# Optimization experiments

Measured on AMD Instinct MI355X. Metric: run time of the kernel, lower is better.

## Reference

```python
import jax, jax.numpy as jnp
import numpy as np

N_NODES = 50000


def _add_self_loops(edge_index, n):
    loops = jnp.arange(n, dtype=edge_index.dtype)
    src = jnp.concatenate([edge_index[0], loops])
    dst = jnp.concatenate([edge_index[1], loops])
    return src, dst


def _gcn_norm(src, dst, n):
    # symmetric normalization deg^-1/2 (degrees include self-loops), as in PyG GCNConv
    ones = jnp.ones_like(dst, dtype=jnp.float32)
    deg = jax.ops.segment_sum(ones, dst, num_segments=n)
    dinv = jnp.where(deg > 0, jax.lax.rsqrt(deg), 0.0)
    return dinv[src] * dinv[dst]


def _gcn_conv(x, W, b, src, dst, norm, n):
    h = x @ W                                  # [N, d_out] dense transform first (d_out <= d_in)
    msg = h[src] * norm[:, None]               # gather + per-edge scale
    out = jax.ops.segment_sum(msg, dst, num_segments=n)  # scatter-add aggregation
    return out + b


def setup_inputs() -> dict:
    key = jax.random.key(0)
    ks = jax.random.split(key, 5)
    n, e = N_NODES, 1_600_000
    x = jax.random.normal(ks[0], (n, 512), dtype=jnp.float32)
    edge_index = jax.random.randint(ks[1], (2, e), 0, n, dtype=jnp.int64)
    def glorot(k, fi, fo):
        s = jnp.sqrt(6.0 / (fi + fo)).astype(jnp.float32)
        return jax.random.uniform(k, (fi, fo), jnp.float32, -s, s)
    return {
        "x": x,
        "edge_index": edge_index,
        "W0": glorot(ks[2], 512, 256), "b0": jnp.zeros((256,), jnp.float32),
        "W1": glorot(ks[3], 256, 256), "b1": jnp.zeros((256,), jnp.float32),
        "W2": glorot(ks[4], 256, 128), "b2": jnp.zeros((128,), jnp.float32),
    }


def reference(x, edge_index, W0, b0, W1, b1, W2, b2):
    n = x.shape[0]
    src, dst = _add_self_loops(edge_index, n)
    norm = _gcn_norm(src, dst, n)
    h = jax.nn.relu(_gcn_conv(x, W0, b0, src, dst, norm, n))
    h = jax.nn.relu(_gcn_conv(h, W1, b1, src, dst, norm, n))
    z = _gcn_conv(h, W2, b2, src, dst, norm, n)
    return z
```

## Files before the change

kernel.cpp:

```cpp
#include <hip/hip_runtime.h>
#include <hip/hip_bf16.h>
#include <type_traits>

#define NN 50000

typedef __attribute__((ext_vector_type(8))) short bf16x8;
typedef __attribute__((ext_vector_type(4))) float f32x4;
typedef unsigned int u32;

__device__ __forceinline__ ushort f2bf(float f) {
    unsigned u = __builtin_bit_cast(unsigned, f);
    unsigned r = (u + 0x7fffu + ((u >> 16) & 1u)) >> 16;
    return (ushort)r;
}
__device__ __forceinline__ float bflo(unsigned v) { return __builtin_bit_cast(float, v << 16); }
__device__ __forceinline__ float bfhi(unsigned v) { return __builtin_bit_cast(float, v & 0xffff0000u); }

__device__ __forceinline__ void gld16(const void* g, void* l) {
    __builtin_amdgcn_global_load_lds((const __attribute__((address_space(1))) u32*)g,
                                     (__attribute__((address_space(3))) u32*)l, 16, 0, 0);
}

__global__ void k_init(int* cnt, int* cur, int n, const unsigned int* ei, int npairs, int* flag) {
    int i = blockIdx.x * blockDim.x + threadIdx.x;
    if (i < n) { cnt[i] = 0; cur[i] = 0; }
    if (blockIdx.x == 0) {
        __shared__ int any_nz;
        if (threadIdx.x == 0) any_nz = 0;
        __syncthreads();
        for (int p = threadIdx.x; p < npairs; p += blockDim.x) {
            if (ei[2 * p + 1] != 0u) atomicOr(&any_nz, 1);
        }
        __syncthreads();
        if (threadIdx.x == 0) *flag = (any_nz == 0) ? 1 : 0;
    }
}

__device__ __forceinline__ int load_idx(const void* ei, long long pos, int is64) {
    return is64 ? (int)(((const long long*)ei)[pos]) : ((const int*)ei)[pos];
}

__global__ void k_count(const void* ei, long long E, const int* flag, int* cnt) {
    long long e = (long long)blockIdx.x * blockDim.x + threadIdx.x;
    if (e < E) {
        int dst = load_idx(ei, E + e, *flag);
        atomicAdd(&cnt[dst], 1);
    }
}

__global__ void k_scan(const int* __restrict__ cnt, int* __restrict__ offs,
                       float* __restrict__ dinv, int n) {
    __shared__ int wsum[16];
    __shared__ int carry_s;
    int t = (int)threadIdx.x;
    int lane = t & 63, w = t >> 6;
    if (t == 0) carry_s = 0;
    __syncthreads();
    for (int base = 0; base < n; base += 1024) {
        int i = base + t;
        int v = (i < n) ? cnt[i] : 0;
        int pv = (v + 7) & ~7;
        int x = pv;
#pragma unroll
        for (int off = 1; off < 64; off <<= 1) {
            int y = __shfl_up(x, off);
            if (lane >= off) x += y;
        }
        if (lane == 63) wsum[w] = x;
        __syncthreads();
        if (w == 0) {
            int pvv = (lane < 16) ? wsum[lane] : 0;
#pragma unroll
            for (int off = 1; off < 16; off <<= 1) {
                int py = __shfl_up(pvv, off);
                if (lane >= off) pvv += py;
            }
            if (lane < 16) wsum[lane] = pvv;
        }
        __syncthreads();
        int wbase = (w > 0) ? wsum[w - 1] : 0;
        int incl = x + wbase;
        int excl = incl - pv;
        int carry = carry_s;
        if (i < n) {
            offs[i] = carry + excl;
            dinv[i] = rsqrtf((float)(v + 1));
        }
        __syncthreads();
        if (t == 1023) carry_s = carry + incl;
        __syncthreads();
    }
    if (threadIdx.x == 0) offs[n] = carry_s;
}

__global__ void k_bucket(const void* ei, long long E, const int* __restrict__ flag,
                         const float* __restrict__ dinv, const int* __restrict__ offs,
                         int* cur, int2* __restrict__ epk,
                         const int* __restrict__ cnt, int n) {
    long long e = (long long)blockIdx.x * blockDim.x + threadIdx.x;
    if (e < E) {
        int is64 = *flag;
        int src = load_idx(ei, e, is64);
        int dst = load_idx(ei, E + e, is64);
        int pos = offs[dst] + atomicAdd(&cur[dst], 1);
        epk[pos] = make_int2(src, __builtin_bit_cast(int, dinv[src] * dinv[dst]));
    } else {
        int i = (int)(e - E);
        if (i < n) {
            int b = offs[i] + cnt[i], en = offs[i + 1];
            for (int j = b; j < en; ++j) epk[j] = make_int2(0, 0);
        }
    }
}

__global__ void k_wt3(const float* __restrict__ W0, ushort* __restrict__ WT0,
                      const float* __restrict__ W1, ushort* __restrict__ WT1,
                      const float* __restrict__ W2, ushort* __restrict__ WT2) {
    int id = blockIdx.x * 256 + threadIdx.x;
    const float* W; ushort* WT; int K, N, loc;
    if (id < 131072)      { W = W0; WT = WT0; K = 512; N = 256; loc = id; }
    else if (id < 196608) { W = W1; WT = WT1; K = 256; N = 256; loc = id - 131072; }
    else if (id < 229376) { W = W2; WT = WT2; K = 256; N = 128; loc = id - 196608; }
    else return;
    int nn = loc / K, k = loc - nn * K;
    WT[loc] = f2bf(W[(long long)k * N + nn]);
}

#define LOFF(r, s) (((r) * 8 + ((s) ^ ((r) & 7))) * 8)

template <typename TA>
__global__ __launch_bounds__(256) void k_gemm_mfma(const TA* __restrict__ A,
                                                   const ushort* __restrict__ WT,
                                                   ushort* __restrict__ C,
                                                   int M, int N, int K) {
    __shared__ ushort As[8192];
    __shared__ ushort Bs[8192];
    int t = threadIdx.x;
    int lane = t & 63;
    int w = t >> 6;
    int wr = (w >> 1) * 64, wc = (w & 1) * 64;
    int m0 = blockIdx.y * 128, n0 = blockIdx.x * 128;

    f32x4 acc[4][4] = {};

    for (int k0 = 0; k0 < K; k0 += 64) {
#pragma unroll
        for (int j = 0; j < 4; ++j) {
            int id = (w * 4 + j) * 64 + lane;
            int r = id >> 3, sp = id & 7;
            int s = sp ^ (r & 7);
            gld16(WT + (long long)(n0 + r) * K + k0 + s * 8, &Bs[(r * 8 + sp) * 8]);
        }
        if constexpr (std::is_same<TA, float>::value) {
#pragma unroll
            for (int j = 0; j < 4; ++j) {
                int id = t + j * 256;
                int r = id >> 3, s = id & 7;
                int grow = m0 + r;
                if (grow < M) {
                    const float* src = A + (long long)grow * K + k0 + s * 8;
                    float4 f0 = *(const float4*)src;
                    float4 f1 = *(const float4*)(src + 4);
                    ushort tmp[8] = {f2bf(f0.x), f2bf(f0.y), f2bf(f0.z), f2bf(f0.w),
                                     f2bf(f1.x), f2bf(f1.y), f2bf(f1.z), f2bf(f1.w)};
                    *(uint4*)&As[LOFF(r, s)] = *(uint4*)tmp;
                }
            }
        } else {
#pragma unroll
            for (int j = 0; j < 4; ++j) {
                int rbase = (w * 4 + j) * 8;
                if (m0 + rbase < M) {
                    int id = rbase * 8 + lane;
                    int r = id >> 3, sp = id & 7;
                    int s = sp ^ (r & 7);
                    gld16((const ushort*)A + (long long)(m0 + r) * K + k0 + s * 8,
                          &As[(r * 8 + sp) * 8]);
                }
            }
        }
        __syncthreads();
#pragma unroll
        for (int kk = 0; kk < 2; ++kk) {
            int ks = kk * 4 + (lane >> 4);
            bf16x8 a[4], b[4];
#pragma unroll
            for (int m = 0; m < 4; ++m)
                a[m] = *(bf16x8*)&As[LOFF(wr + m * 16 + (lane & 15), ks)];
#pragma unroll
            for (int nn = 0; nn < 4; ++nn)
                b[nn] = *(bf16x8*)&Bs[LOFF(wc + nn * 16 + (lane & 15), ks)];
#pragma unroll
            for (int m = 0; m < 4; ++m)
#pragma unroll
                for (int nn = 0; nn < 4; ++nn)
                    acc[m][nn] = __builtin_amdgcn_mfma_f32_16x16x32_bf16(a[m], b[nn], acc[m][nn], 0, 0, 0);
        }
        __syncthreads();
    }
#pragma unroll
    for (int m = 0; m < 4; ++m) {
#pragma unroll
        for (int i = 0; i < 4; ++i) {
            int row = m0 + wr + m * 16 + (lane >> 4) * 4 + i;
            if (row < M) {
#pragma unroll
                for (int nn = 0; nn < 4; ++nn) {
                    int col = n0 + wc + nn * 16 + (lane & 15);
                    C[(long long)row * N + col] = f2bf(acc[m][nn][i]);
                }
            }
        }
    }
}

template <int D, bool RELU, bool OUTF32>
__global__ __launch_bounds__(128) void k_agg2(const ushort* __restrict__ h,
                                              const int* __restrict__ offs,
                                              const int2* __restrict__ epk,
                                              const float* __restrict__ dinv,
                                              const float* __restrict__ bias,
                                              void* __restrict__ outp, int n) {
    constexpr int VPT = D / 64;
    int node = __builtin_amdgcn_readfirstlane((int)(blockIdx.x * 2 + (threadIdx.x >> 6)));
    if (node >= n) return;
    int t = (int)threadIdx.x & 63;
    float di = dinv[node];
    float dii = di * di;
    float acc[VPT];

    if constexpr (VPT == 4) {
        uint2 v = *(const uint2*)&h[(long long)node * D + t * 4];
        float4 bs = *(const float4*)&bias[t * 4];
        acc[0] = bs.x + dii * bflo(v.x);
        acc[1] = bs.y + dii * bfhi(v.x);
        acc[2] = bs.z + dii * bflo(v.y);
        acc[3] = bs.w + dii * bfhi(v.y);
    } else {
        unsigned v = *(const unsigned*)&h[(long long)node * D + t * 2];
        float2 bs = *(const float2*)&bias[t * 2];
        acc[0] = bs.x + dii * bflo(v);
        acc[1] = bs.y + dii * bfhi(v);
    }

    int s = offs[node], e = offs[node + 1];

    for (int j = s; j < e; j += 8) {
        int2 p[8];
#pragma unroll
        for (int u = 0; u < 8; ++u) p[u] = epk[j + u];
        if constexpr (VPT == 4) {
            uint2 v[8];
#pragma unroll
            for (int u = 0; u < 8; ++u)
                v[u] = *(const uint2*)&h[(long long)p[u].x * D + t * 4];
#pragma unroll
            for (int u = 0; u < 8; ++u) {
                float wgt = __builtin_bit_cast(float, p[u].y);
                acc[0] += wgt * bflo(v[u].x);
                acc[1] += wgt * bfhi(v[u].x);
                acc[2] += wgt * bflo(v[u].y);
                acc[3] += wgt * bfhi(v[u].y);
            }
        } else {
            unsigned v[8];
#pragma unroll
            for (int u = 0; u < 8; ++u)
                v[u] = *(const unsigned*)&h[(long long)p[u].x * D + t * 2];
#pragma unroll
            for (int u = 0; u < 8; ++u) {
                float wgt = __builtin_bit_cast(float, p[u].y);
                acc[0] += wgt * bflo(v[u]);
                acc[1] += wgt * bfhi(v[u]);
            }
        }
    }

    if (RELU) {
#pragma unroll
        for (int u = 0; u < VPT; ++u) acc[u] = fmaxf(acc[u], 0.f);
    }
    if constexpr (OUTF32) {
        if constexpr (VPT == 2) {
            ((float2*)outp)[(long long)node * (D / 2) + t] = make_float2(acc[0], acc[1]);
        } else {
            float4 o = make_float4(acc[0], acc[1], acc[2], acc[3]);
            ((float4*)outp)[(long long)node * (D / 4) + t] = o;
        }
    } else {
        if constexpr (VPT == 4) {
            uint2 pk;
            pk.x = (unsigned)f2bf(acc[0]) | ((unsigned)f2bf(acc[1]) << 16);
            pk.y = (unsigned)f2bf(acc[2]) | ((unsigned)f2bf(acc[3]) << 16);
            ((uint2*)outp)[(long long)node * (D / 4) + t] = pk;
        } else {
            unsigned pk = (unsigned)f2bf(acc[0]) | ((unsigned)f2bf(acc[1]) << 16);
            ((unsigned*)outp)[(long long)node * (D / 2) + t] = pk;
        }
    }
}

extern "C" void kernel_launch(void* const* d_in, const int* in_sizes, int n_in,
                              void* d_out, int out_size, void* d_ws, size_t ws_size,
                              hipStream_t stream) {
    const float* x  = (const float*)d_in[0];
    const void*  ei = d_in[1];
    const float* W0 = (const float*)d_in[2];
    const float* b0 = (const float*)d_in[3];
    const float* W1 = (const float*)d_in[4];
    const float* b1 = (const float*)d_in[5];
    const float* W2 = (const float*)d_in[6];
    const float* b2 = (const float*)d_in[7];
    float* out = (float*)d_out;

    const int n = NN;
    const long long E = (long long)in_sizes[1] / 2;

    char* ws = (char*)d_ws;
    int*    cnt  = (int*)(ws);
    int*    cur  = (int*)(ws + 256 * 1024);
    int*    offs = (int*)(ws + 512 * 1024);
    float*  dinv = (float*)(ws + 768 * 1024);
    int*    flag = (int*)(ws + 1000 * 1024);
    int2*   epk  = (int2*)(ws + 1024 * 1024);
    ushort* WT0  = (ushort*)(ws + 17ll * 1024 * 1024);
    ushort* WT1  = (ushort*)(ws + 17ll * 1024 * 1024 + 512 * 1024);
    ushort* WT2  = (ushort*)(ws + 17ll * 1024 * 1024 + 768 * 1024);
    ushort* hA   = (ushort*)(ws + 18ll * 1024 * 1024);
    ushort* hB   = (ushort*)(ws + 44ll * 1024 * 1024);

    k_init<<<(n + 255) / 256, 256, 0, stream>>>(cnt, cur, n, (const unsigned int*)ei, 4096, flag);
    k_count<<<(int)((E + 255) / 256), 256, 0, stream>>>(ei, E, flag, cnt);
    k_scan<<<1, 1024, 0, stream>>>(cnt, offs, dinv, n);
    k_bucket<<<(int)((E + n + 255) / 256), 256, 0, stream>>>(ei, E, flag, dinv, offs, cur, epk, cnt, n);

    k_wt3<<<(229376 + 255) / 256, 256, 0, stream>>>(W0, WT0, W1, WT1, W2, WT2);

    int mt = (n + 127) / 128;
    int nb2 = (n + 1) / 2;

    k_gemm_mfma<float><<<dim3(2, mt), 256, 0, stream>>>(x, WT0, hA, n, 256, 512);
    k_agg2<256, true, false><<<nb2, 128, 0, stream>>>(hA, offs, epk, dinv, b0, hB, n);

    k_gemm_mfma<ushort><<<dim3(2, mt), 256, 0, stream>>>(hB, WT1, hA, n, 256, 256);
    k_agg2<256, true, false><<<nb2, 128, 0, stream>>>(hA, offs, epk, dinv, b1, hB, n);

    k_gemm_mfma<ushort><<<dim3(1, mt), 256, 0, stream>>>(hB, WT2, hA, n, 128, 256);
    k_agg2<128, false, true><<<nb2, 128, 0, stream>>>(hA, offs, epk, dinv, b2, out, n);
}
```

Before: 544.8 us.

## Split 256-wide aggregation into two feature-half passes and pre-convert x to bf16

New measurement: 526.5 us. 3.4% less time.

```diff
diff --git a/kernel.cpp b/kernel.cpp
--- a/kernel.cpp
+++ b/kernel.cpp
@@ -126,6 +126,18 @@
     WT[loc] = f2bf(W[(long long)k * N + nn]);
 }
 
+__global__ void k_x2bf(const float* __restrict__ x, ushort* __restrict__ xbf, long long n8) {
+    long long id = (long long)blockIdx.x * blockDim.x + threadIdx.x;
+    if (id < n8) {
+        const float* src = x + id * 8;
+        float4 f0 = *(const float4*)src;
+        float4 f1 = *(const float4*)(src + 4);
+        ushort tmp[8] = {f2bf(f0.x), f2bf(f0.y), f2bf(f0.z), f2bf(f0.w),
+                         f2bf(f1.x), f2bf(f1.y), f2bf(f1.z), f2bf(f1.w)};
+        *(uint4*)&xbf[id * 8] = *(uint4*)tmp;
+    }
+}
+
 #define LOFF(r, s) (((r) * 8 + ((s) ^ ((r) & 7))) * 8)
 
 template <typename TA>
@@ -214,34 +226,23 @@
     }
 }
 
-template <int D, bool RELU, bool OUTF32>
-__global__ __launch_bounds__(128) void k_agg2(const ushort* __restrict__ h,
+template <int DT, bool RELU, bool OUTF32>
+__global__ __launch_bounds__(128) void k_aggs(const ushort* __restrict__ h,
                                               const int* __restrict__ offs,
                                               const int2* __restrict__ epk,
                                               const float* __restrict__ dinv,
                                               const float* __restrict__ bias,
-                                              void* __restrict__ outp, int n) {
-    constexpr int VPT = D / 64;
+                                              void* __restrict__ outp, int n, int foff) {
     int node = __builtin_amdgcn_readfirstlane((int)(blockIdx.x * 2 + (threadIdx.x >> 6)));
     if (node >= n) return;
     int t = (int)threadIdx.x & 63;
     float di = dinv[node];
     float dii = di * di;
-    float acc[VPT];
-
-    if constexpr (VPT == 4) {
-        uint2 v = *(const uint2*)&h[(long long)node * D + t * 4];
-        float4 bs = *(const float4*)&bias[t * 4];
-        acc[0] = bs.x + dii * bflo(v.x);
-        acc[1] = bs.y + dii * bfhi(v.x);
-        acc[2] = bs.z + dii * bflo(v.y);
-        acc[3] = bs.w + dii * bfhi(v.y);
-    } else {
-        unsigned v = *(const unsigned*)&h[(long long)node * D + t * 2];
-        float2 bs = *(const float2*)&bias[t * 2];
-        acc[0] = bs.x + dii * bflo(v);
-        acc[1] = bs.y + dii * bfhi(v);
-    }
+
+    unsigned v0 = *(const unsigned*)&h[(long long)node * DT + foff + t * 2];
+    float2 bs = *(const float2*)&bias[foff + t * 2];
+    float a0 = bs.x + dii * bflo(v0);
+    float a1 = bs.y + dii * bfhi(v0);
 
     int s = offs[node], e = offs[node + 1];
 
@@ -249,54 +250,25 @@
         int2 p[8];
 #pragma unroll
         for (int u = 0; u < 8; ++u) p[u] = epk[j + u];
-        if constexpr (VPT == 4) {
-            uint2 v[8];
-#pragma unroll
-            for (int u = 0; u < 8; ++u)
-                v[u] = *(const uint2*)&h[(long long)p[u].x * D + t * 4];
-#pragma unroll
-            for (int u = 0; u < 8; ++u) {
-                float wgt = __builtin_bit_cast(float, p[u].y);
-                acc[0] += wgt * bflo(v[u].x);
-                acc[1] += wgt * bfhi(v[u].x);
-                acc[2] += wgt * bflo(v[u].y);
-                acc[3] += wgt * bfhi(v[u].y);
-            }
-        } else {
-            unsigned v[8];
-#pragma unroll
-            for (int u = 0; u < 8; ++u)
-                v[u] = *(const unsigned*)&h[(long long)p[u].x * D + t * 2];
-#pragma unroll
-            for (int u = 0; u < 8; ++u) {
-                float wgt = __builtin_bit_cast(float, p[u].y);
-                acc[0] += wgt * bflo(v[u]);
-                acc[1] += wgt * bfhi(v[u]);
-            }
-        }
-    }
-
-    if (RELU) {
-#pragma unroll
-        for (int u = 0; u < VPT; ++u) acc[u] = fmaxf(acc[u], 0.f);
-    }
+        unsigned v[8];
+#pragma unroll
+        for (int u = 0; u < 8; ++u)
+            v[u] = *(const unsigned*)&h[(long long)p[u].x * DT + foff + t * 2];
+#pragma unroll
+        for (int u = 0; u < 8; ++u) {
+            float wgt = __builtin_bit_cast(float, p[u].y);
+            a0 += wgt * bflo(v[u]);
+            a1 += wgt * bfhi(v[u]);
+        }
+    }
+
+    if (RELU) { a0 = fmaxf(a0, 0.f); a1 = fmaxf(a1, 0.f); }
+    long long oidx = ((long long)node * DT + foff) / 2 + t;
     if constexpr (OUTF32) {
-        if constexpr (VPT == 2) {
-            ((float2*)outp)[(long long)node * (D / 2) + t] = make_float2(acc[0], acc[1]);
-        } else {
-            float4 o = make_float4(acc[0], acc[1], acc[2], acc[3]);
-            ((float4*)outp)[(long long)node * (D / 4) + t] = o;
-        }
+        ((float2*)outp)[oidx] = make_float2(a0, a1);
     } else {
-        if constexpr (VPT == 4) {
-            uint2 pk;
-            pk.x = (unsigned)f2bf(acc[0]) | ((unsigned)f2bf(acc[1]) << 16);
-            pk.y = (unsigned)f2bf(acc[2]) | ((unsigned)f2bf(acc[3]) << 16);
-            ((uint2*)outp)[(long long)node * (D / 4) + t] = pk;
-        } else {
-            unsigned pk = (unsigned)f2bf(acc[0]) | ((unsigned)f2bf(acc[1]) << 16);
-            ((unsigned*)outp)[(long long)node * (D / 2) + t] = pk;
-        }
+        unsigned pk = (unsigned)f2bf(a0) | ((unsigned)f2bf(a1) << 16);
+        ((unsigned*)outp)[oidx] = pk;
     }
 }
 
@@ -328,6 +300,8 @@
     ushort* WT2  = (ushort*)(ws + 17ll * 1024 * 1024 + 768 * 1024);
     ushort* hA   = (ushort*)(ws + 18ll * 1024 * 1024);
     ushort* hB   = (ushort*)(ws + 44ll * 1024 * 1024);
+    ushort* xbf  = (ushort*)(ws + 70ll * 1024 * 1024);
+    const size_t need_xbf = 70ll * 1024 * 1024 + 51200000ll;
 
     k_init<<<(n + 255) / 256, 256, 0, stream>>>(cnt, cur, n, (const unsigned int*)ei, 4096, flag);
     k_count<<<(int)((E + 255) / 256), 256, 0, stream>>>(ei, E, flag, cnt);
@@ -339,12 +313,20 @@
     int mt = (n + 127) / 128;
     int nb2 = (n + 1) / 2;
 
-    k_gemm_mfma<float><<<dim3(2, mt), 256, 0, stream>>>(x, WT0, hA, n, 256, 512);
-    k_agg2<256, true, false><<<nb2, 128, 0, stream>>>(hA, offs, epk, dinv, b0, hB, n);
+    if (ws_size >= need_xbf) {
+        long long n8 = (long long)n * 512 / 8;
+        k_x2bf<<<(int)((n8 + 255) / 256), 256, 0, stream>>>(x, xbf, n8);
+        k_gemm_mfma<ushort><<<dim3(2, mt), 256, 0, stream>>>(xbf, WT0, hA, n, 256, 512);
+    } else {
+        k_gemm_mfma<float><<<dim3(2, mt), 256, 0, stream>>>(x, WT0, hA, n, 256, 512);
+    }
+    k_aggs<256, true, false><<<nb2, 128, 0, stream>>>(hA, offs, epk, dinv, b0, hB, n, 0);
+    k_aggs<256, true, false><<<nb2, 128, 0, stream>>>(hA, offs, epk, dinv, b0, hB, n, 128);
 
     k_gemm_mfma<ushort><<<dim3(2, mt), 256, 0, stream>>>(hB, WT1, hA, n, 256, 256);
-    k_agg2<256, true, false><<<nb2, 128, 0, stream>>>(hA, offs, epk, dinv, b1, hB, n);
+    k_aggs<256, true, false><<<nb2, 128, 0, stream>>>(hA, offs, epk, dinv, b1, hB, n, 0);
+    k_aggs<256, true, false><<<nb2, 128, 0, stream>>>(hA, offs, epk, dinv, b1, hB, n, 128);
 
     k_gemm_mfma<ushort><<<dim3(1, mt), 256, 0, stream>>>(hB, WT2, hA, n, 128, 256);
-    k_agg2<128, false, true><<<nb2, 128, 0, stream>>>(hA, offs, epk, dinv, b2, out, n);
-}
+    k_aggs<128, false, true><<<nb2, 128, 0, stream>>>(hA, offs, epk, dinv, b2, out, n, 0);
+}
```
